# Kernel tuning notes

Measured on AMD Instinct MI355X. Metric: run time of the kernel, lower is better.

Reference implementation:

```python
import jax, jax.numpy as jnp
import numpy as np

B, CIN, COUT, K, H, W, DLAT = 16, 512, 512, 3, 64, 64, 512
EPS = 1e-8

def setup_inputs() -> dict:
    key = jax.random.key(0)
    ks = jax.random.split(key, 9)
    return {
        "x": jax.random.normal(ks[0], (B, CIN, H, W), jnp.float32),
        "s": jax.random.normal(ks[1], (B, DLAT), jnp.float32),
        "map_w0": jax.random.normal(ks[2], (DLAT, DLAT), jnp.float32),
        "map_b0": jax.random.normal(ks[3], (DLAT,), jnp.float32),
        "prelu_a0": jnp.full((DLAT,), 0.25, jnp.float32),  # torch PReLU default init
        "map_w1": jax.random.normal(ks[4], (DLAT, DLAT), jnp.float32),
        "map_b1": jax.random.normal(ks[5], (DLAT,), jnp.float32),
        "prelu_a1": jnp.full((DLAT,), 0.25, jnp.float32),
        "style_w": jax.random.normal(ks[6], (CIN, DLAT), jnp.float32),
        "style_b": jax.random.normal(ks[7], (CIN,), jnp.float32),
        "conv_w": jax.random.normal(ks[8], (COUT, CIN, K, K), jnp.float32),
    }

def _prelu(z, a):
    return jnp.where(z >= 0, z, a * z)

def reference(x, s, map_w0, map_b0, prelu_a0, map_w1, map_b1, prelu_a1, style_w, style_b, conv_w):
    c_lin = np.float32(1.0 / np.sqrt(DLAT))  # equalized-LR scale 1/sqrt(fan_in)
    # to_style: MappingNetwork (2 layers) + final EqualizedLinear
    z = _prelu(s @ (map_w0 * c_lin).T + map_b0, prelu_a0)
    z = _prelu(z @ (map_w1 * c_lin).T + map_b1, prelu_a1)
    style = z @ (style_w * c_lin).T + style_b  # [B, CIN]
    # modulate per-sample weights
    c_conv = np.float32(1.0 / np.sqrt(CIN * K * K))
    w = (conv_w * c_conv)[None] * style[:, None, :, None, None]  # [B, COUT, CIN, K, K]
    # demodulate
    sigma_inv = jax.lax.rsqrt(jnp.sum(w * w, axis=(2, 3, 4), keepdims=True) + EPS)
    w = w * sigma_inv
    # replication (edge) pad by (K-1)//2, then per-sample VALID conv (== grouped conv with groups=B)
    pad = (K - 1) // 2
    x_pad = jnp.pad(x, ((0, 0), (0, 0), (pad, pad), (pad, pad)), mode="edge")

    def per_sample(xi, wi):  # xi [CIN,Hp,Wp], wi [COUT,CIN,K,K]
        return jax.lax.conv_general_dilated(
            xi[None], wi, window_strides=(1, 1), padding="VALID",
            dimension_numbers=("NCHW", "OIHW", "NCHW"))[0]

    return jax.vmap(per_sample)(x_pad, w)  # [B, COUT, H, W]
```

## Files before the change

kernel.cpp:

```cpp
#include <hip/hip_runtime.h>

typedef unsigned short ushort_t;
typedef unsigned int uint_t;
typedef __attribute__((ext_vector_type(8))) short bhalf8;
typedef __attribute__((ext_vector_type(4))) float f32x4;

#define C_LIN  0.04419417382415922f
#define C_CONV 0.014731391274719738f

__device__ __forceinline__ ushort_t f2bf(float f) {
    uint_t u = __float_as_uint(f);
    u += 0x7fffu + ((u >> 16) & 1u);
    return (ushort_t)(u >> 16);
}

__device__ __forceinline__ void gload16(const void* g, void* l) {
    __builtin_amdgcn_global_load_lds((const __attribute__((address_space(1))) void*)g,
                                     (__attribute__((address_space(3))) void*)l, 16, 0, 0);
}

__global__ void map_layer_k(const float* __restrict__ zin, const float* __restrict__ w,
                            const float* __restrict__ bias, const float* __restrict__ alpha,
                            float* __restrict__ zout, int final_) {
    __shared__ float zs[512];
    const int b = blockIdx.y, tid = threadIdx.x;
    if (tid < 128) ((float4*)zs)[tid] = ((const float4*)(zin + b * 512))[tid];
    __syncthreads();
    const int j = blockIdx.x * 64 + (tid >> 2);
    const int part = (tid & 3) * 128;
    const float4* wr = (const float4*)(w + (size_t)j * 512 + part);
    const float* zp = zs + part;
    float acc = 0.f;
#pragma unroll 8
    for (int i = 0; i < 32; ++i) {
        float4 w4 = wr[i];
        acc += w4.x * zp[4*i] + w4.y * zp[4*i+1] + w4.z * zp[4*i+2] + w4.w * zp[4*i+3];
    }
    acc += __shfl_xor(acc, 1);
    acc += __shfl_xor(acc, 2);
    if ((tid & 3) == 0) {
        acc = acc * C_LIN + bias[j];
        if (final_) acc *= C_CONV;
        else        acc = acc >= 0.f ? acc : alpha[j] * acc;
        zout[b * 512 + j] = acc;
    }
}

__global__ void wsqbf_k(const float* __restrict__ cw, float* __restrict__ wsq,
                        ushort_t* __restrict__ wbf2) {
    int idx = blockIdx.x * 256 + threadIdx.x;
    int cout = idx >> 9, ci = idx & 511;
    const float* p = cw + (size_t)idx * 9;
    float v[9], sum = 0.f;
#pragma unroll
    for (int k = 0; k < 9; ++k) { v[k] = p[k]; sum += v[k] * v[k]; }
    wsq[idx] = sum;
    const size_t base = ((size_t)(((cout >> 6) * 16 + (ci >> 5)) * 4 + ((cout >> 4) & 3))) * 512
                        + (((ci >> 3) & 3) * 16 + (cout & 15)) * 8 + (ci & 7);
#pragma unroll
    for (int k = 0; k < 9; ++k)
        wbf2[(size_t)k * 262144 + base] = f2bf(v[k]);
}

__global__ void sigma_k(const float* __restrict__ style_c, const float* __restrict__ wsq,
                        float* __restrict__ sig) {
    __shared__ float s2[512];
    const int b = blockIdx.y, cb = blockIdx.x, tid = threadIdx.x;
    if (tid < 128) {
        float4 sv = ((const float4*)(style_c + b * 512))[tid];
        s2[4*tid]   = sv.x * sv.x; s2[4*tid+1] = sv.y * sv.y;
        s2[4*tid+2] = sv.z * sv.z; s2[4*tid+3] = sv.w * sv.w;
    }
    __syncthreads();
    const int c = cb * 32 + (tid >> 3);
    const int part = (tid & 7) * 64;
    const float4* wr = (const float4*)(wsq + (size_t)c * 512 + part);
    const float* zp = s2 + part;
    float acc = 0.f;
#pragma unroll
    for (int i = 0; i < 16; ++i) {
        float4 w = wr[i];
        acc += w.x * zp[4*i] + w.y * zp[4*i+1] + w.z * zp[4*i+2] + w.w * zp[4*i+3];
    }
    acc += __shfl_xor(acc, 1);
    acc += __shfl_xor(acc, 2);
    acc += __shfl_xor(acc, 4);
    if ((tid & 7) == 0) sig[b * 512 + c] = 1.0f / sqrtf(acc + 1e-8f);
}

__global__ void xmod_k(const float* __restrict__ x, const float* __restrict__ style_c,
                       ushort_t* __restrict__ xm) {
    const int y = blockIdx.x, b = blockIdx.y, tid = threadIdx.x;
    const float* xp = x + ((size_t)b * 512) * 4096 + y * 64;
    ushort_t* op = xm + (((size_t)b * 64 + y) * 64) * 512;
    __shared__ ushort_t tile[32][68];
    for (int cin0 = 0; cin0 < 512; cin0 += 32) {
#pragma unroll
        for (int t = 0; t < 2; ++t) {
            int i = tid + t * 256;
            int ci = i >> 4, x4 = i & 15;
            float4 v = *(const float4*)(xp + (size_t)(cin0 + ci) * 4096 + x4 * 4);
            float sc = style_c[b * 512 + cin0 + ci];
            tile[ci][x4*4]   = f2bf(v.x * sc); tile[ci][x4*4+1] = f2bf(v.y * sc);
            tile[ci][x4*4+2] = f2bf(v.z * sc); tile[ci][x4*4+3] = f2bf(v.w * sc);
        }
        __syncthreads();
#pragma unroll
        for (int t = 0; t < 4; ++t) {
            int i = tid + t * 256;
            int xc = i >> 4, c2 = i & 15;
            ushort2 pr;
            pr.x = tile[c2*2][xc]; pr.y = tile[c2*2+1][xc];
            *(ushort2*)(op + (size_t)xc * 512 + cin0 + c2 * 2) = pr;
        }
        __syncthreads();
    }
}

template <bool XPRE>
__global__ __launch_bounds__(256, 2)
void conv_k(const float* __restrict__ x, const ushort_t* __restrict__ xm,
            const ushort_t* __restrict__ wbf2, const float* __restrict__ style_c,
            const float* __restrict__ sig, float* __restrict__ out) {
    __shared__ __align__(16) ushort_t xs[21504];

    const int tid  = threadIdx.x;
    const int lane = tid & 63;
    const int wv   = tid >> 6;
    const int l15  = lane & 15, l4 = lane >> 4;

    const int bid = blockIdx.x;
    const int swz = (bid & 7) * 128 + (bid >> 3);
    const int b     = swz >> 6;
    const int cout0 = ((swz >> 3) & 7) * 64;
    const int r0    = (swz & 7) * 8;

    const int nx = (wv < 2) ? 11 : 10;

    int gxo[11];
#pragma unroll
    for (int t = 0; t < 11; ++t) {
        if (t < nx) {
            int L = (wv + 4 * t) * 64 + lane;
            int k = (L >> 3) & 3, s = L & 7;
            int p = ((L >> 5) << 3) | ((s ^ (k * 2)) & 7);
            p = min(p, 659);
            int row = p / 66, col = p - row * 66;
            int gy = min(max(r0 - 1 + row, 0), 63);
            int gx = min(max(col - 1, 0), 63);
            gxo[t] = (((b * 64 + gy) * 64 + gx) << 9) + k * 8;
        } else gxo[t] = 0;
    }

    const ushort_t* wbase = wbf2 + (size_t)(cout0 >> 6) * 16 * 4 * 512 + lane * 8;

    f32x4 acc[2][4][4] = {};

    for (int c0 = 0; c0 < 512; c0 += 32) {
        __syncthreads();
        if (XPRE) {
#pragma unroll
            for (int t = 0; t < 11; ++t)
                if (t < nx)
                    gload16(xm + gxo[t] + c0, (char*)xs + (wv + 4 * t) * 1024);
        } else {
#pragma unroll
            for (int t = 0; t < 11; ++t) {
                if (t < nx) {
                    int L = (wv + 4 * t) * 64 + lane;
                    int k = (L >> 3) & 3, s = L & 7;
                    int p = ((L >> 5) << 3) | ((s ^ (k * 2)) & 7);
                    p = min(p, 659);
                    int row = p / 66, col = p - row * 66;
                    int gy = min(max(r0 - 1 + row, 0), 63);
                    int gx = min(max(col - 1, 0), 63);
                    const float* xp = x + ((size_t)(b * 512 + c0 + k * 8)) * 4096 + gy * 64 + gx;
                    const float* sc = style_c + b * 512 + c0 + k * 8;
                    ushort_t tmp[8];
#pragma unroll
                    for (int e = 0; e < 8; ++e)
                        tmp[e] = f2bf(xp[(size_t)e * 4096] * sc[e]);
                    *(bhalf8*)((char*)xs + (size_t)L * 16) = *(const bhalf8*)tmp;
                }
            }
        }
        asm volatile("s_waitcnt vmcnt(0)" ::: "memory");
        __syncthreads();

        const ushort_t* wk = wbase + (size_t)(c0 >> 5) * 4 * 512;

#pragma unroll
        for (int dx = 0; dx < 3; ++dx) {
            bhalf8 af[3][4];
#pragma unroll
            for (int dy = 0; dy < 3; ++dy)
#pragma unroll
                for (int m = 0; m < 4; ++m)
                    af[dy][m] = *(const bhalf8*)(wk + ((size_t)(dy * 3 + dx) * 8 * 16 * 4 + m) * 512);
#pragma unroll
            for (int ri = 0; ri < 4; ++ri) {
                const int p0 = (wv * 2 + ri) * 66 + dx + l15;
                const int bb = (p0 >> 3) * 512 + l4 * 128 + (((p0 & 7) ^ (l4 * 2)) & 7) * 16;
                bhalf8 bfr[4];
#pragma unroll
                for (int n = 0; n < 4; ++n)
                    bfr[n] = *(const bhalf8*)((const char*)xs + bb + n * 1024);
#pragma unroll
                for (int dy = 0; dy < 3; ++dy) {
                    const int r_out = ri - dy;
                    if (r_out < 0 || r_out > 1) continue;
#pragma unroll
                    for (int m = 0; m < 4; ++m)
#pragma unroll
                        for (int n = 0; n < 4; ++n)
                            acc[r_out][m][n] = __builtin_amdgcn_mfma_f32_16x16x32_bf16(
                                af[dy][m], bfr[n], acc[r_out][m][n], 0, 0, 0);
                }
            }
        }
    }

#pragma unroll
    for (int r_out = 0; r_out < 2; ++r_out) {
        const int orow = r0 + wv * 2 + r_out;
#pragma unroll
        for (int m = 0; m < 4; ++m) {
#pragma unroll
            for (int r = 0; r < 4; ++r) {
                int cout = cout0 + m * 16 + l4 * 4 + r;
                float sg = sig[b * 512 + cout];
                float* op = out + (((size_t)b * 512 + cout) * 64 + orow) * 64;
#pragma unroll
                for (int n = 0; n < 4; ++n)
                    op[n * 16 + l15] = acc[r_out][m][n][r] * sg;
            }
        }
    }
}

extern "C" void kernel_launch(void* const* d_in, const int* in_sizes, int n_in,
                              void* d_out, int out_size, void* d_ws, size_t ws_size,
                              hipStream_t stream) {
    const float* x  = (const float*)d_in[0];
    const float* s  = (const float*)d_in[1];
    const float* w0 = (const float*)d_in[2];
    const float* b0 = (const float*)d_in[3];
    const float* a0 = (const float*)d_in[4];
    const float* w1 = (const float*)d_in[5];
    const float* b1 = (const float*)d_in[6];
    const float* a1 = (const float*)d_in[7];
    const float* sw = (const float*)d_in[8];
    const float* sb = (const float*)d_in[9];
    const float* cw = (const float*)d_in[10];
    float* out = (float*)d_out;

    float*    style_c = (float*)d_ws;
    float*    sig     = style_c + 8192;
    float*    zt0     = sig + 8192;
    float*    zt1     = zt0 + 8192;
    float*    wsq     = zt1 + 8192;
    ushort_t* wbf2    = (ushort_t*)(wsq + 262144);
    ushort_t* xm      = (ushort_t*)((char*)d_ws + 5898240);
    const bool xpre = ws_size >= 73007104ull;

    wsqbf_k<<<1024, 256, 0, stream>>>(cw, wsq, wbf2);
    map_layer_k<<<dim3(8, 16), 256, 0, stream>>>(s,   w0, b0, a0, zt0,     0);
    map_layer_k<<<dim3(8, 16), 256, 0, stream>>>(zt0, w1, b1, a1, zt1,     0);
    map_layer_k<<<dim3(8, 16), 256, 0, stream>>>(zt1, sw, sb, a1, style_c, 1);
    sigma_k<<<dim3(16, 16), 256, 0, stream>>>(style_c, wsq, sig);
    if (xpre) {
        xmod_k<<<dim3(64, 16), 256, 0, stream>>>(x, style_c, xm);
        conv_k<true><<<1024, 256, 0, stream>>>(x, xm, wbf2, style_c, sig, out);
    } else {
        conv_k<false><<<1024, 256, 0, stream>>>(x, xm, wbf2, style_c, sig, out);
    }
}
```

Measured before the change: 323.6 us.

## Double-buffer weight and input tiles in LDS for the conv kernel

The conv kernel now stages both the bf16 weight slices and the modulated input tile into LDS with double buffering, prefetching the next 32-channel chunk while the current one feeds the MFMAs. Before, weights were read directly from global memory into registers and the input tile was loaded synchronously. The weight prep kernel now writes a plain [tap][cout][cin] layout, and the swizzle is applied during the LDS load. LDS use grows to about 160 KB, so launch bounds drop to one block per CU, which trades occupancy for overlap of loads with compute.

```diff
diff --git a/kernel.cpp b/kernel.cpp
--- a/kernel.cpp
+++ b/kernel.cpp
@@ -47,19 +47,16 @@
 }
 
 __global__ void wsqbf_k(const float* __restrict__ cw, float* __restrict__ wsq,
-                        ushort_t* __restrict__ wbf2) {
+                        ushort_t* __restrict__ wbf) {
     int idx = blockIdx.x * 256 + threadIdx.x;
-    int cout = idx >> 9, ci = idx & 511;
     const float* p = cw + (size_t)idx * 9;
     float v[9], sum = 0.f;
 #pragma unroll
     for (int k = 0; k < 9; ++k) { v[k] = p[k]; sum += v[k] * v[k]; }
     wsq[idx] = sum;
-    const size_t base = ((size_t)(((cout >> 6) * 16 + (ci >> 5)) * 4 + ((cout >> 4) & 3))) * 512
-                        + (((ci >> 3) & 3) * 16 + (cout & 15)) * 8 + (ci & 7);
 #pragma unroll
     for (int k = 0; k < 9; ++k)
-        wbf2[(size_t)k * 262144 + base] = f2bf(v[k]);
+        wbf[(size_t)k * 262144 + idx] = f2bf(v[k]);
 }
 
 __global__ void sigma_k(const float* __restrict__ style_c, const float* __restrict__ wsq,
@@ -118,11 +115,12 @@
 }
 
 template <bool XPRE>
-__global__ __launch_bounds__(256, 2)
+__global__ __launch_bounds__(256, 1)
 void conv_k(const float* __restrict__ x, const ushort_t* __restrict__ xm,
-            const ushort_t* __restrict__ wbf2, const float* __restrict__ style_c,
+            const ushort_t* __restrict__ wbf, const float* __restrict__ style_c,
             const float* __restrict__ sig, float* __restrict__ out) {
-    __shared__ __align__(16) ushort_t xs[21504];
+    __shared__ __align__(16) ushort_t wt[2][18432];
+    __shared__ __align__(16) ushort_t xs[2][21504];
 
     const int tid  = threadIdx.x;
     const int lane = tid & 63;
@@ -137,6 +135,14 @@
 
     const int nx = (wv < 2) ? 11 : 10;
 
+    int gw[9];
+#pragma unroll
+    for (int t = 0; t < 9; ++t) {
+        int L = (wv * 9 + t) * 64 + lane;
+        int tap = L >> 8, win = (L >> 5) & 7, k = (L >> 3) & 3, s = L & 7;
+        int c = win * 8 + ((s ^ (k * 2)) & 7);
+        gw[t] = ((tap * 512 + cout0 + c) << 9) + k * 8;
+    }
     int gxo[11];
 #pragma unroll
     for (int t = 0; t < 11; ++t) {
@@ -152,17 +158,18 @@
         } else gxo[t] = 0;
     }
 
-    const ushort_t* wbase = wbf2 + (size_t)(cout0 >> 6) * 16 * 4 * 512 + lane * 8;
-
     f32x4 acc[2][4][4] = {};
-
-    for (int c0 = 0; c0 < 512; c0 += 32) {
-        __syncthreads();
+    const int base_af = (l15 >> 3) * 512 + l4 * 128 + (((l15 & 7) ^ (l4 * 2)) & 7) * 16;
+
+    auto stage = [&](int c0, int pb) {
+#pragma unroll
+        for (int t = 0; t < 9; ++t)
+            gload16(wbf + gw[t] + c0, (char*)wt[pb] + (wv * 9 + t) * 1024);
         if (XPRE) {
 #pragma unroll
             for (int t = 0; t < 11; ++t)
                 if (t < nx)
-                    gload16(xm + gxo[t] + c0, (char*)xs + (wv + 4 * t) * 1024);
+                    gload16(xm + gxo[t] + c0, (char*)xs[pb] + (wv + 4 * t) * 1024);
         } else {
 #pragma unroll
             for (int t = 0; t < 11; ++t) {
@@ -180,14 +187,22 @@
 #pragma unroll
                     for (int e = 0; e < 8; ++e)
                         tmp[e] = f2bf(xp[(size_t)e * 4096] * sc[e]);
-                    *(bhalf8*)((char*)xs + (size_t)L * 16) = *(const bhalf8*)tmp;
+                    *(bhalf8*)((char*)xs[pb] + (size_t)L * 16) = *(const bhalf8*)tmp;
                 }
             }
         }
-        asm volatile("s_waitcnt vmcnt(0)" ::: "memory");
-        __syncthreads();
-
-        const ushort_t* wk = wbase + (size_t)(c0 >> 5) * 4 * 512;
+    };
+
+    stage(0, 0);
+    asm volatile("s_waitcnt vmcnt(0)" ::: "memory");
+    __syncthreads();
+
+    for (int it = 0; it < 16; ++it) {
+        const int cur = it & 1;
+        if (it < 15) stage((it + 1) * 32, cur ^ 1);
+
+        const char* wtc = (const char*)wt[cur];
+        const char* xsc = (const char*)xs[cur];
 
 #pragma unroll
         for (int dx = 0; dx < 3; ++dx) {
@@ -196,7 +211,7 @@
             for (int dy = 0; dy < 3; ++dy)
 #pragma unroll
                 for (int m = 0; m < 4; ++m)
-                    af[dy][m] = *(const bhalf8*)(wk + ((size_t)(dy * 3 + dx) * 8 * 16 * 4 + m) * 512);
+                    af[dy][m] = *(const bhalf8*)(wtc + base_af + (dy * 3 + dx) * 4096 + m * 1024);
 #pragma unroll
             for (int ri = 0; ri < 4; ++ri) {
                 const int p0 = (wv * 2 + ri) * 66 + dx + l15;
@@ -204,7 +219,7 @@
                 bhalf8 bfr[4];
 #pragma unroll
                 for (int n = 0; n < 4; ++n)
-                    bfr[n] = *(const bhalf8*)((const char*)xs + bb + n * 1024);
+                    bfr[n] = *(const bhalf8*)(xsc + bb + n * 1024);
 #pragma unroll
                 for (int dy = 0; dy < 3; ++dy) {
                     const int r_out = ri - dy;
@@ -218,6 +233,8 @@
                 }
             }
         }
+        asm volatile("s_waitcnt vmcnt(0)" ::: "memory");
+        __syncthreads();
     }
 
 #pragma unroll
@@ -259,19 +276,19 @@
     float*    zt0     = sig + 8192;
     float*    zt1     = zt0 + 8192;
     float*    wsq     = zt1 + 8192;
-    ushort_t* wbf2    = (ushort_t*)(wsq + 262144);
+    ushort_t* wbf     = (ushort_t*)(wsq + 262144);
     ushort_t* xm      = (ushort_t*)((char*)d_ws + 5898240);
     const bool xpre = ws_size >= 73007104ull;
 
-    wsqbf_k<<<1024, 256, 0, stream>>>(cw, wsq, wbf2);
+    wsqbf_k<<<1024, 256, 0, stream>>>(cw, wsq, wbf);
     map_layer_k<<<dim3(8, 16), 256, 0, stream>>>(s,   w0, b0, a0, zt0,     0);
     map_layer_k<<<dim3(8, 16), 256, 0, stream>>>(zt0, w1, b1, a1, zt1,     0);
     map_layer_k<<<dim3(8, 16), 256, 0, stream>>>(zt1, sw, sb, a1, style_c, 1);
     sigma_k<<<dim3(16, 16), 256, 0, stream>>>(style_c, wsq, sig);
     if (xpre) {
         xmod_k<<<dim3(64, 16), 256, 0, stream>>>(x, style_c, xm);
-        conv_k<true><<<1024, 256, 0, stream>>>(x, xm, wbf2, style_c, sig, out);
+        conv_k<true><<<1024, 256, 0, stream>>>(x, xm, wbf, style_c, sig, out);
     } else {
-        conv_k<false><<<1024, 256, 0, stream>>>(x, xm, wbf2, style_c, sig, out);
-    }
-}
+        conv_k<false><<<1024, 256, 0, stream>>>(x, xm, wbf, style_c, sig, out);
+    }
+}
```

New measurement: 378.2 us. +16.9%, slower.

## Stage conv weights into LDS via async global_load_lds with swizzled layout

Applied to the files above, without the earlier changes.

The bf16 conv weights get a new layout: blocked by 32-channel chunk, then tap, then cout. Each c0 iteration now copies the block's 9-tap 64x32 weight tile into a new LDS buffer with global_load_lds, and the MFMA A fragments are read from LDS through an XOR swizzle. Before, each wave fetched those fragments directly from global memory. The change also adds an s_sleep to stagger half of the blocks, and it raises LDS use per block by about 36KB, which can limit occupancy.

```diff
diff --git a/kernel.cpp b/kernel.cpp
--- a/kernel.cpp
+++ b/kernel.cpp
@@ -47,7 +47,7 @@
 }
 
 __global__ void wsqbf_k(const float* __restrict__ cw, float* __restrict__ wsq,
-                        ushort_t* __restrict__ wbf2) {
+                        ushort_t* __restrict__ wbf3) {
     int idx = blockIdx.x * 256 + threadIdx.x;
     int cout = idx >> 9, ci = idx & 511;
     const float* p = cw + (size_t)idx * 9;
@@ -55,11 +55,10 @@
 #pragma unroll
     for (int k = 0; k < 9; ++k) { v[k] = p[k]; sum += v[k] * v[k]; }
     wsq[idx] = sum;
-    const size_t base = ((size_t)(((cout >> 6) * 16 + (ci >> 5)) * 4 + ((cout >> 4) & 3))) * 512
-                        + (((ci >> 3) & 3) * 16 + (cout & 15)) * 8 + (ci & 7);
+    const size_t base = (size_t)(ci >> 5) * 9 * 16384 + cout * 32 + (ci & 31);
 #pragma unroll
     for (int k = 0; k < 9; ++k)
-        wbf2[(size_t)k * 262144 + base] = f2bf(v[k]);
+        wbf3[base + (size_t)k * 16384] = f2bf(v[k]);
 }
 
 __global__ void sigma_k(const float* __restrict__ style_c, const float* __restrict__ wsq,
@@ -120,8 +119,9 @@
 template <bool XPRE>
 __global__ __launch_bounds__(256, 2)
 void conv_k(const float* __restrict__ x, const ushort_t* __restrict__ xm,
-            const ushort_t* __restrict__ wbf2, const float* __restrict__ style_c,
+            const ushort_t* __restrict__ wbf3, const float* __restrict__ style_c,
             const float* __restrict__ sig, float* __restrict__ out) {
+    __shared__ __align__(16) ushort_t wt[18432];
     __shared__ __align__(16) ushort_t xs[21504];
 
     const int tid  = threadIdx.x;
@@ -135,8 +135,18 @@
     const int cout0 = ((swz >> 3) & 7) * 64;
     const int r0    = (swz & 7) * 8;
 
+    if ((bid >> 8) & 1) __builtin_amdgcn_s_sleep(60);
+
     const int nx = (wv < 2) ? 11 : 10;
 
+    int gw[9];
+#pragma unroll
+    for (int t = 0; t < 9; ++t) {
+        int L = (wv * 9 + t) * 64 + lane;
+        int tap = L >> 8, win = (L >> 5) & 7, k = (L >> 3) & 3, s = L & 7;
+        int c = win * 8 + ((s ^ (k * 2)) & 7);
+        gw[t] = tap * 16384 + (cout0 + c) * 32 + k * 8;
+    }
     int gxo[11];
 #pragma unroll
     for (int t = 0; t < 11; ++t) {
@@ -152,12 +162,15 @@
         } else gxo[t] = 0;
     }
 
-    const ushort_t* wbase = wbf2 + (size_t)(cout0 >> 6) * 16 * 4 * 512 + lane * 8;
-
     f32x4 acc[2][4][4] = {};
+    const int base_af = (l15 >> 3) * 512 + l4 * 128 + (((l15 & 7) ^ (l4 * 2)) & 7) * 16;
 
     for (int c0 = 0; c0 < 512; c0 += 32) {
-        __syncthreads();
+        const int wco = (c0 >> 5) * 147456;
+        __syncthreads();
+#pragma unroll
+        for (int t = 0; t < 9; ++t)
+            gload16(wbf3 + gw[t] + wco, (char*)wt + (wv * 9 + t) * 1024);
         if (XPRE) {
 #pragma unroll
             for (int t = 0; t < 11; ++t)
@@ -187,8 +200,6 @@
         asm volatile("s_waitcnt vmcnt(0)" ::: "memory");
         __syncthreads();
 
-        const ushort_t* wk = wbase + (size_t)(c0 >> 5) * 4 * 512;
-
 #pragma unroll
         for (int dx = 0; dx < 3; ++dx) {
             bhalf8 af[3][4];
@@ -196,7 +207,7 @@
             for (int dy = 0; dy < 3; ++dy)
 #pragma unroll
                 for (int m = 0; m < 4; ++m)
-                    af[dy][m] = *(const bhalf8*)(wk + ((size_t)(dy * 3 + dx) * 8 * 16 * 4 + m) * 512);
+                    af[dy][m] = *(const bhalf8*)((const char*)wt + base_af + (dy * 3 + dx) * 4096 + m * 1024);
 #pragma unroll
             for (int ri = 0; ri < 4; ++ri) {
                 const int p0 = (wv * 2 + ri) * 66 + dx + l15;
@@ -259,19 +270,19 @@
     float*    zt0     = sig + 8192;
     float*    zt1     = zt0 + 8192;
     float*    wsq     = zt1 + 8192;
-    ushort_t* wbf2    = (ushort_t*)(wsq + 262144);
+    ushort_t* wbf3    = (ushort_t*)(wsq + 262144);
     ushort_t* xm      = (ushort_t*)((char*)d_ws + 5898240);
     const bool xpre = ws_size >= 73007104ull;
 
-    wsqbf_k<<<1024, 256, 0, stream>>>(cw, wsq, wbf2);
+    wsqbf_k<<<1024, 256, 0, stream>>>(cw, wsq, wbf3);
     map_layer_k<<<dim3(8, 16), 256, 0, stream>>>(s,   w0, b0, a0, zt0,     0);
     map_layer_k<<<dim3(8, 16), 256, 0, stream>>>(zt0, w1, b1, a1, zt1,     0);
     map_layer_k<<<dim3(8, 16), 256, 0, stream>>>(zt1, sw, sb, a1, style_c, 1);
     sigma_k<<<dim3(16, 16), 256, 0, stream>>>(style_c, wsq, sig);
     if (xpre) {
         xmod_k<<<dim3(64, 16), 256, 0, stream>>>(x, style_c, xm);
-        conv_k<true><<<1024, 256, 0, stream>>>(x, xm, wbf2, style_c, sig, out);
+        conv_k<true><<<1024, 256, 0, stream>>>(x, xm, wbf3, style_c, sig, out);
     } else {
-        conv_k<false><<<1024, 256, 0, stream>>>(x, xm, wbf2, style_c, sig, out);
-    }
-}
+        conv_k<false><<<1024, 256, 0, stream>>>(x, xm, wbf3, style_c, sig, out);
+    }
+}
```

Result: faster. 301.5 us (-6.8%).
